# Performance work log

Hardware: AMD Instinct MI355X
Metric: run time of the kernel (lower is better)

## Reference

```python
import jax, jax.numpy as jnp
import numpy as np

GRADIENT_SCALE = 1.0  # undefined global in the source; standard surrogate scale
ALPHA = 0.9
BETA = 0.8
THRESHOLD = 1.0
FEATURES = 512
UNITS = 1024
TIME = 256
BATCH = 128

@jax.custom_vjp
def heaviside(x):
    return jnp.where(x > 0, jnp.ones_like(x), jnp.zeros_like(x))

def _heaviside_fwd(x):
    return heaviside(x), x

def _heaviside_bwd(x, dy):
    # dy * GRADIENT_SCALE * (1/(|x|+1))^2  (surrogate gradient from tf.custom_gradient)
    return (dy * (GRADIENT_SCALE * jnp.square(1.0 / (jnp.abs(x) + 1.0))),)

heaviside.defvjp(_heaviside_fwd, _heaviside_bwd)


def setup_inputs() -> dict:
    key = jax.random.key(0)
    k1, k2 = jax.random.split(key)
    inputs = jax.random.normal(k1, (BATCH, FEATURES, TIME), dtype=jnp.float32)
    # keras add_weight default initializer ~ glorot_uniform; any float init is fine for a numerics baseline
    limit = np.sqrt(6.0 / (FEATURES + UNITS)).astype(np.float32)
    w = jax.random.uniform(k2, (FEATURES, UNITS), dtype=jnp.float32, minval=-limit, maxval=limit)
    return {"inputs": inputs, "w": w}


def reference(inputs, w):
    # In the original tf.while_loop body, membrane_potential, synapse and prev_s are
    # returned UNMODIFIED, so they remain zero for every timestep. The recurrence
    # therefore collapses exactly to, per step t:
    #   h_t = x[:, :, t] @ w
    #   i_t = alpha*0 + h_t = h_t
    #   v_t = (beta*0 + h_t) * (threshold - 0) = h_t * threshold
    #   s_t = heaviside(v_t - threshold)
    # which is timestep-independent and can be computed as one batched GEMM.
    h = jnp.einsum('bft,fu->btu', inputs, w)        # [B, T, U]
    v = (BETA * 0.0 + h) * (THRESHOLD - 0.0)        # state terms are identically zero
    s = heaviside(v - THRESHOLD)                    # [B, T, U]
    return jnp.transpose(s, (0, 2, 1))              # [B, U, T], matching tf transpose perm=[1,2,0]
```

## Files before the change

kernel.cpp:

```cpp
#include <hip/hip_runtime.h>


#define BB 128
#define FF 512
#define TT 256
#define UU 1024

__global__ __launch_bounds__(256, 4)
void snn_gemm_kernel(const float* __restrict__ in, const float* __restrict__ w,
                     float* __restrict__ out) {
    __shared__ float As[16][128];
    __shared__ float Bs[16][128];

    const int b  = blockIdx.z;
    const int u0 = blockIdx.y * 128;
    const int t0 = blockIdx.x * 128;

    const float* __restrict__ inb  = in  + (size_t)b * FF * TT;
    float* __restrict__       outb = out + (size_t)b * UU * TT;

    const int tid = threadIdx.x;
    const int tx  = tid & 15;
    const int ty  = tid >> 4;

    const int k0 = tid >> 5;
    const int c0 = (tid & 31) * 4;
    const int k1 = k0 + 8;

    float acc[8][8];
#pragma unroll
    for (int i = 0; i < 8; i++)
#pragma unroll
        for (int j = 0; j < 8; j++) acc[i][j] = 0.0f;

    float4 a_r0 = *(const float4*)&w[(size_t)k0 * UU + u0 + c0];
    float4 a_r1 = *(const float4*)&w[(size_t)k1 * UU + u0 + c0];
    float4 b_r0 = *(const float4*)&inb[k0 * TT + t0 + c0];
    float4 b_r1 = *(const float4*)&inb[k1 * TT + t0 + c0];

    for (int f0 = 0; f0 < FF; f0 += 16) {
        *(float4*)&As[k0][c0] = a_r0;
        *(float4*)&As[k1][c0] = a_r1;
        *(float4*)&Bs[k0][c0] = b_r0;
        *(float4*)&Bs[k1][c0] = b_r1;
        __syncthreads();

        if (f0 + 16 < FF) {
            const int fn = f0 + 16;
            a_r0 = *(const float4*)&w[(size_t)(fn + k0) * UU + u0 + c0];
            a_r1 = *(const float4*)&w[(size_t)(fn + k1) * UU + u0 + c0];
            b_r0 = *(const float4*)&inb[(fn + k0) * TT + t0 + c0];
            b_r1 = *(const float4*)&inb[(fn + k1) * TT + t0 + c0];
        }

#pragma unroll
        for (int k = 0; k < 16; k++) {
            const float4 a0 = *(const float4*)&As[k][ty * 4];
            const float4 a1 = *(const float4*)&As[k][ty * 4 + 64];
            const float4 v0 = *(const float4*)&Bs[k][tx * 4];
            const float4 v1 = *(const float4*)&Bs[k][tx * 4 + 64];
            const float am[8] = {a0.x, a0.y, a0.z, a0.w, a1.x, a1.y, a1.z, a1.w};
            const float bn[8] = {v0.x, v0.y, v0.z, v0.w, v1.x, v1.y, v1.z, v1.w};
#pragma unroll
            for (int i = 0; i < 8; i++)
#pragma unroll
                for (int j = 0; j < 8; j++)
                    acc[i][j] = fmaf(am[i], bn[j], acc[i][j]);
        }
        __syncthreads();
    }

#pragma unroll
    for (int i = 0; i < 8; i++) {
        const int m = (i < 4) ? (ty * 4 + i) : (64 + ty * 4 + i - 4);
        float* __restrict__ orow = outb + (size_t)(u0 + m) * TT + t0;
        float4 o0, o1;
        o0.x = acc[i][0] > 1.0f ? 1.0f : 0.0f;
        o0.y = acc[i][1] > 1.0f ? 1.0f : 0.0f;
        o0.z = acc[i][2] > 1.0f ? 1.0f : 0.0f;
        o0.w = acc[i][3] > 1.0f ? 1.0f : 0.0f;
        o1.x = acc[i][4] > 1.0f ? 1.0f : 0.0f;
        o1.y = acc[i][5] > 1.0f ? 1.0f : 0.0f;
        o1.z = acc[i][6] > 1.0f ? 1.0f : 0.0f;
        o1.w = acc[i][7] > 1.0f ? 1.0f : 0.0f;
        *(float4*)&orow[tx * 4]      = o0;
        *(float4*)&orow[tx * 4 + 64] = o1;
    }
}

extern "C" void kernel_launch(void* const* d_in, const int* in_sizes, int n_in,
                              void* d_out, int out_size, void* d_ws, size_t ws_size,
                              hipStream_t stream) {
    const float* in = (const float*)d_in[0];
    const float* w  = (const float*)d_in[1];
    float* out      = (float*)d_out;

    dim3 grid(TT / 128, UU / 128, BB);
    snn_gemm_kernel<<<grid, dim3(256), 0, stream>>>(in, w, out);
}
```

Baseline: 553.0 us.

## Use split-bf16 MFMA GEMM with transpose prepass and exact fp32 fallback near threshold

Adds a prepass that transposes inputs and weights and splits each fp32 value into high and low bf16 parts. The main kernel then runs three bf16 MFMA products (hi*hi, hi*lo, lo*hi) with global-to-LDS direct loads in place of the scalar fp32 FMA GEMM. Outputs whose accumulated value lies within 1e-3 of the threshold are recomputed exactly in fp32, so the thresholded spikes should stay correct. The cost is extra workspace traffic for the prepass and possible divergence in the fallback path. The old kernel remains as a fallback when the workspace is too small.

```diff
diff --git a/kernel.cpp b/kernel.cpp
--- a/kernel.cpp
+++ b/kernel.cpp
@@ -5,6 +5,174 @@
 #define FF 512
 #define TT 256
 #define UU 1024
+
+typedef float v4f __attribute__((ext_vector_type(4)));
+typedef short v8s __attribute__((ext_vector_type(8)));
+
+__device__ __forceinline__ unsigned short bf16rn(float x) {
+    unsigned u = __float_as_uint(x);
+    u = u + 0x7FFFu + ((u >> 16) & 1u);
+    return (unsigned short)(u >> 16);
+}
+__device__ __forceinline__ float bf16tof(unsigned short h) {
+    return __uint_as_float(((unsigned)h) << 16);
+}
+
+__global__ __launch_bounds__(256)
+void prepass_kernel(const float* __restrict__ in, const float* __restrict__ w,
+                    unsigned short* __restrict__ xth, unsigned short* __restrict__ xtl,
+                    unsigned short* __restrict__ wth, unsigned short* __restrict__ wtl) {
+    __shared__ float Ls[64][65];
+
+    const int z = blockIdx.z;
+    const float* src;
+    int srow;
+    unsigned short *dh, *dl;
+    if (z < BB) {
+        src = in + (size_t)z * FF * TT;  srow = TT;
+        dh = xth + (size_t)z * TT * FF;  dl = xtl + (size_t)z * TT * FF;
+    } else {
+        const int s = z - BB;
+        src = w + s * 256;               srow = UU;
+        dh = wth + (size_t)s * 256 * FF; dl = wtl + (size_t)s * 256 * FF;
+    }
+    const int f0 = blockIdx.y * 64;
+    const int c0 = blockIdx.x * 64;
+    const int tid = threadIdx.x;
+    const int r  = tid >> 4;
+    const int c4 = (tid & 15) * 4;
+
+#pragma unroll
+    for (int i = 0; i < 4; i++) {
+        const float4 v = *(const float4*)&src[(size_t)(f0 + r + 16 * i) * srow + c0 + c4];
+        Ls[r + 16 * i][c4 + 0] = v.x;
+        Ls[r + 16 * i][c4 + 1] = v.y;
+        Ls[r + 16 * i][c4 + 2] = v.z;
+        Ls[r + 16 * i][c4 + 3] = v.w;
+    }
+    __syncthreads();
+
+#pragma unroll
+    for (int i = 0; i < 4; i++) {
+        const int orow = r + 16 * i;
+        float a0 = Ls[c4 + 0][orow];
+        float a1 = Ls[c4 + 1][orow];
+        float a2 = Ls[c4 + 2][orow];
+        float a3 = Ls[c4 + 3][orow];
+        unsigned short h0 = bf16rn(a0), h1 = bf16rn(a1), h2 = bf16rn(a2), h3 = bf16rn(a3);
+        float l0f = a0 - bf16tof(h0);
+        float l1f = a1 - bf16tof(h1);
+        float l2f = a2 - bf16tof(h2);
+        float l3f = a3 - bf16tof(h3);
+        unsigned short l0 = bf16rn(l0f), l1 = bf16rn(l1f), l2 = bf16rn(l2f), l3 = bf16rn(l3f);
+        unsigned long long hp = (unsigned long long)h0 | ((unsigned long long)h1 << 16)
+                              | ((unsigned long long)h2 << 32) | ((unsigned long long)h3 << 48);
+        unsigned long long lp = (unsigned long long)l0 | ((unsigned long long)l1 << 16)
+                              | ((unsigned long long)l2 << 32) | ((unsigned long long)l3 << 48);
+        const size_t o = (size_t)(c0 + orow) * FF + f0 + c4;
+        *(unsigned long long*)&dh[o] = hp;
+        *(unsigned long long*)&dl[o] = lp;
+    }
+}
+
+#define GLL(g, l) __builtin_amdgcn_global_load_lds(                     \
+    (const __attribute__((address_space(1))) void*)(g),                 \
+    (__attribute__((address_space(3))) void*)(l), 16, 0, 0)
+
+__global__ __launch_bounds__(256)
+void snn_mfma_kernel(const unsigned short* __restrict__ wth,
+                     const unsigned short* __restrict__ wtl,
+                     const unsigned short* __restrict__ xth,
+                     const unsigned short* __restrict__ xtl,
+                     const float* __restrict__ in, const float* __restrict__ w,
+                     float* __restrict__ out) {
+    __shared__ unsigned short smem[4 * 128 * 32];
+
+    const int b  = blockIdx.z;
+    const int u0 = blockIdx.y * 128;
+    const int t0 = blockIdx.x * 128;
+
+    const int tid = threadIdx.x;
+    const int wv  = tid >> 6;
+    const int ln  = tid & 63;
+    const int lr  = ln & 15;
+    const int lq  = ln >> 4;
+    const int wm  = (wv & 1) * 64;
+    const int wn  = (wv >> 1) * 64;
+
+    const char* gbase;
+    if      (wv == 0) gbase = (const char*)wth + (size_t)u0 * (FF * 2);
+    else if (wv == 1) gbase = (const char*)wtl + (size_t)u0 * (FF * 2);
+    else if (wv == 2) gbase = (const char*)xth + ((size_t)b * TT + t0) * (FF * 2);
+    else              gbase = (const char*)xtl + ((size_t)b * TT + t0) * (FF * 2);
+    const int lrow = ln >> 2;
+    const int lseg = (ln & 3) * 16;
+
+    unsigned short* lbase = &smem[wv * 4096];
+
+    v4f acc[4][4];
+#pragma unroll
+    for (int i = 0; i < 4; i++)
+#pragma unroll
+        for (int j = 0; j < 4; j++) {
+            v4f zz = {0.0f, 0.0f, 0.0f, 0.0f};
+            acc[i][j] = zz;
+        }
+
+    for (int f0 = 0; f0 < FF; f0 += 32) {
+#pragma unroll
+        for (int s = 0; s < 8; s++) {
+            const char* ga = gbase + (size_t)(s * 16 + lrow) * (FF * 2) + f0 * 2 + lseg;
+            GLL(ga, (char*)lbase + s * 1024);
+        }
+        __syncthreads();
+
+#pragma unroll
+        for (int p = 0; p < 3; p++) {
+            const unsigned short* Ap = &smem[(p == 2 ? 1 : 0) * 4096];
+            const unsigned short* Bp = &smem[(p == 1 ? 3 : 2) * 4096];
+            v8s af[4], bfr[4];
+#pragma unroll
+            for (int i = 0; i < 4; i++)
+                af[i] = *(const v8s*)&Ap[(wm + i * 16 + lr) * 32 + lq * 8];
+#pragma unroll
+            for (int j = 0; j < 4; j++)
+                bfr[j] = *(const v8s*)&Bp[(wn + j * 16 + lr) * 32 + lq * 8];
+#pragma unroll
+            for (int i = 0; i < 4; i++)
+#pragma unroll
+                for (int j = 0; j < 4; j++)
+                    acc[i][j] = __builtin_amdgcn_mfma_f32_16x16x32_bf16(
+                        af[i], bfr[j], acc[i][j], 0, 0, 0);
+        }
+        __syncthreads();
+    }
+
+    const float* xb   = in  + (size_t)b * FF * TT;
+    float* __restrict__ outb = out + (size_t)b * UU * TT;
+#pragma unroll
+    for (int i = 0; i < 4; i++) {
+#pragma unroll
+        for (int r = 0; r < 4; r++) {
+            const int u = u0 + wm + i * 16 + lq * 4 + r;
+#pragma unroll
+            for (int j = 0; j < 4; j++) {
+                const int t = t0 + wn + j * 16 + lr;
+                float h = acc[i][j][r];
+                if (__builtin_expect(__builtin_fabsf(h - 1.0f) <= 1e-3f, 0)) {
+                    float s2 = 0.0f;
+                    const float* wp = w  + u;
+                    const float* xp = xb + t;
+#pragma unroll 16
+                    for (int f = 0; f < FF; f++)
+                        s2 = fmaf(wp[(size_t)f * UU], xp[(size_t)f * TT], s2);
+                    h = s2;
+                }
+                outb[(size_t)u * TT + t] = h > 1.0f ? 1.0f : 0.0f;
+            }
+        }
+    }
+}
 
 __global__ __launch_bounds__(256, 4)
 void snn_gemm_kernel(const float* __restrict__ in, const float* __restrict__ w,
@@ -95,6 +263,19 @@
     const float* w  = (const float*)d_in[1];
     float* out      = (float*)d_out;
 
-    dim3 grid(TT / 128, UU / 128, BB);
-    snn_gemm_kernel<<<grid, dim3(256), 0, stream>>>(in, w, out);
-}
+    const size_t XN  = (size_t)BB * TT * FF;
+    const size_t WN  = (size_t)UU * FF;
+    const size_t NEED = (2 * XN + 2 * WN) * sizeof(unsigned short);
+
+    if (ws_size >= NEED) {
+        unsigned short* xth = (unsigned short*)d_ws;
+        unsigned short* xtl = xth + XN;
+        unsigned short* wth = xtl + XN;
+        unsigned short* wtl = wth + WN;
+        prepass_kernel<<<dim3(4, 8, 132), dim3(256), 0, stream>>>(in, w, xth, xtl, wth, wtl);
+        snn_mfma_kernel<<<dim3(TT / 128, UU / 128, BB), dim3(256), 0, stream>>>(
+            wth, wtl, xth, xtl, in, w, out);
+    } else {
+        snn_gemm_kernel<<<dim3(TT / 128, UU / 128, BB), dim3(256), 0, stream>>>(in, w, out);
+    }
+}
```

Result: slower. 615.9 us (+11.4%).
